# Optimization experiments

Measured on AMD Instinct MI355X. Metric: run time of the kernel, lower is better.

The kernel has to match this reference:

```python
import jax, jax.numpy as jnp
import numpy as np

B, S, D, H = 8, 1024, 1024, 16
DK = D // H
NEG = -1e9


def setup_inputs() -> dict:
    key = jax.random.key(0)
    ks = jax.random.split(key, 11)
    s = 1.0 / np.sqrt(D)
    inp = {
        "query": jax.random.normal(ks[0], (B, S, D), jnp.float32),
        "key": jax.random.normal(ks[1], (B, S, D), jnp.float32),
        "value": jax.random.normal(ks[2], (B, S, D), jnp.float32),
        "mask": jnp.tril(jnp.ones((S, S), jnp.int32))[None, None],  # causal [1,1,S,S]
        "w_q": jax.random.normal(ks[3], (D, D), jnp.float32) * s,
        "b_q": jnp.zeros((D,), jnp.float32),
        "w_k": jax.random.normal(ks[4], (D, D), jnp.float32) * s,
        "b_k": jnp.zeros((D,), jnp.float32),
        "w_v": jax.random.normal(ks[5], (D, D), jnp.float32) * s,
        "b_v": jnp.zeros((D,), jnp.float32),
        "w_o": jax.random.normal(ks[6], (D, D), jnp.float32) * s,
        "b_o": jnp.zeros((D,), jnp.float32),
    }
    return inp


def reference(query, key, value, mask, w_q, b_q, w_k, b_k, w_v, b_v, w_o, b_o):
    # projections; weights stored as [in, out] (torch Linear applies x @ W.T; here
    # we use x @ W which is the same math with W = torch_W.T)
    def proj(x, w, b):
        # [B,S,D] -> [B,H,S,DK]
        y = x @ w + b
        return y.reshape(B, S, H, DK).transpose(0, 2, 1, 3)

    q = proj(query, w_q, b_q)
    k = proj(key, w_k, b_k)
    v = proj(value, w_v, b_v)

    scores = jnp.einsum("bhqd,bhkd->bhqk", q, k) / jnp.sqrt(jnp.float32(DK))
    scores = jnp.where(mask == 0, jnp.float32(NEG), scores)
    probs = jax.nn.softmax(scores, axis=-1)
    # dropout: eval mode (identity) for deterministic reference
    ctx = jnp.einsum("bhqk,bhkd->bhqd", probs, v)
    ctx = ctx.transpose(0, 2, 1, 3).reshape(B, S, D)
    return ctx @ w_o + b_o
```

## Files before the change

kernel.cpp:

```cpp
#include <hip/hip_runtime.h>

#define B_ 8
#define S_ 1024
#define D_ 1024
#define H_ 16
#define DK_ 64
#define M_ (B_ * S_)
#define NEGINF -1e38f

typedef __bf16 bf16_t;
typedef __bf16 bf16x8 __attribute__((ext_vector_type(8)));
typedef float f32x4 __attribute__((ext_vector_type(4)));
typedef unsigned int u32;

__device__ inline f32x4 mfma_bf16(bf16x8 a, bf16x8 b, f32x4 c) {
    return __builtin_amdgcn_mfma_f32_16x16x32_bf16(a, b, c, 0, 0, 0);
}

typedef const __attribute__((address_space(1))) u32* gas1_t;
typedef __attribute__((address_space(3))) u32* las3_t;
__device__ inline void gl_lds16(const void* g, void* l) {
    __builtin_amdgcn_global_load_lds((gas1_t)g, (las3_t)l, 16, 0, 0);
}

__device__ inline bf16x8 load8(const bf16_t* p) { return *(const bf16x8*)p; }
__device__ inline bf16x8 load8(const float* p) {
    const f32x4 a = *(const f32x4*)p;
    const f32x4 b = *(const f32x4*)(p + 4);
    bf16x8 r;
    r[0] = (bf16_t)a[0]; r[1] = (bf16_t)a[1];
    r[2] = (bf16_t)a[2]; r[3] = (bf16_t)a[3];
    r[4] = (bf16_t)b[0]; r[5] = (bf16_t)b[1];
    r[6] = (bf16_t)b[2]; r[7] = (bf16_t)b[3];
    return r;
}
__device__ inline void store_elem(bf16_t* Y, size_t i, float v) { Y[i] = (bf16_t)v; }
__device__ inline void store_elem(float* Y, size_t i, float v) { Y[i] = v; }

__global__ __launch_bounds__(256) void transpose4(
    const float* __restrict__ i0, const float* __restrict__ i1,
    const float* __restrict__ i2, const float* __restrict__ i3,
    bf16_t* __restrict__ o0, bf16_t* __restrict__ o1,
    bf16_t* __restrict__ o2, bf16_t* __restrict__ o3) {
    const float* ins[4] = {i0, i1, i2, i3};
    bf16_t* outs[4] = {o0, o1, o2, o3};
    const float* in = ins[blockIdx.z];
    bf16_t* out = outs[blockIdx.z];
    __shared__ __align__(16) bf16_t t[32][33];
    const int n0 = blockIdx.x * 32, k0 = blockIdx.y * 32;
    const int tx = threadIdx.x;
    for (int i = threadIdx.y; i < 32; i += 8)
        t[i][tx] = (bf16_t)in[(size_t)(k0 + i) * D_ + n0 + tx];
    __syncthreads();
    for (int i = threadIdx.y; i < 32; i += 8)
        out[(size_t)(n0 + i) * D_ + k0 + tx] = t[tx][i];
}

__global__ __launch_bounds__(256) void cvt_bf16(const float* __restrict__ in,
                                                bf16_t* __restrict__ out,
                                                int n8) {
    const int i = blockIdx.x * 256 + threadIdx.x;
    if (i < n8) *(bf16x8*)(out + (size_t)i * 8) = load8(in + (size_t)i * 8);
}

template <int MODE, typename TX, typename TY>
__global__ __launch_bounds__(256) void gemm_bt(
    const TX* __restrict__ X, const bf16_t* __restrict__ Wt,
    const float* __restrict__ bias, TY* __restrict__ Y, float scale) {
    __shared__ __align__(16) bf16_t As[2][128 * 64];
    __shared__ __align__(16) bf16_t Bs[2][128 * 64];
    const int tid = threadIdx.x;
    const int lane = tid & 63, wave = tid >> 6;
    const int ln = lane & 15, quad = lane >> 4;
    const int wm = (wave & 1) * 64, wn = (wave >> 1) * 64;
    const int m0 = blockIdx.x * 128, n0 = blockIdx.y * 128;

    const int srow = tid >> 3;
    const int sch = tid & 7;
    const int swc = sch ^ (srow & 7);

    const TX* pa = X + (size_t)(m0 + srow) * D_ + swc * 8;
    const bf16_t* pb = Wt + (size_t)(n0 + srow) * D_ + swc * 8;

    auto stage = [&](int d, int k0) {
        if constexpr (sizeof(TX) == 2) {
#pragma unroll
            for (int i = 0; i < 4; i++)
                gl_lds16(pa + (size_t)(i * 32) * D_ + k0,
                         As[d] + i * 2048 + wave * 512);
        } else {
#pragma unroll
            for (int i = 0; i < 4; i++)
                *(bf16x8*)(As[d] + (srow + i * 32) * 64 + sch * 8) =
                    load8(X + (size_t)(m0 + srow + i * 32) * D_ + k0 + swc * 8);
        }
#pragma unroll
        for (int i = 0; i < 4; i++)
            gl_lds16(pb + (size_t)(i * 32) * D_ + k0,
                     Bs[d] + i * 2048 + wave * 512);
    };

    stage(0, 0);
    __syncthreads();

    f32x4 acc[4][4] = {};
    int cur = 0;
    for (int t = 0; t < 16; ++t) {
        if (t < 15) stage(cur ^ 1, (t + 1) * 64);
#pragma unroll
        for (int kq = 0; kq < 2; kq++) {
            bf16x8 af[4], bfr[4];
            const int slot = ((kq * 4 + quad) ^ (ln & 7)) * 8;
#pragma unroll
            for (int mt = 0; mt < 4; mt++)
                af[mt] =
                    *(const bf16x8*)(As[cur] + (wm + mt * 16 + ln) * 64 + slot);
#pragma unroll
            for (int nt = 0; nt < 4; nt++)
                bfr[nt] =
                    *(const bf16x8*)(Bs[cur] + (wn + nt * 16 + ln) * 64 + slot);
#pragma unroll
            for (int mt = 0; mt < 4; mt++)
#pragma unroll
                for (int nt = 0; nt < 4; nt++)
                    acc[mt][nt] = mfma_bf16(af[mt], bfr[nt], acc[mt][nt]);
        }
        __syncthreads();
        cur ^= 1;
    }

#pragma unroll
    for (int mt = 0; mt < 4; mt++) {
#pragma unroll
        for (int nt = 0; nt < 4; nt++) {
#pragma unroll
            for (int r = 0; r < 4; r++) {
                const int m = m0 + wm + mt * 16 + quad * 4 + r;
                const int n = n0 + wn + nt * 16 + ln;
                const float v = (acc[mt][nt][r] + bias[n]) * scale;
                size_t idx;
                if (MODE == 0) {
                    idx = (size_t)m * D_ + n;
                } else {
                    const int b = m >> 10, s = m & 1023;
                    const int h = n >> 6, d = n & 63;
                    if (MODE == 1)
                        idx = ((size_t)(b * H_ + h) * S_ + s) * DK_ + d;
                    else
                        idx = ((size_t)(b * H_ + h) * DK_ + d) * S_ + s;
                }
                store_elem(Y, idx, v);
            }
        }
    }
}

__global__ __launch_bounds__(256, 4) void MaskedMultiHeadAttention_90709709291709_kernel(
    const bf16_t* __restrict__ Q, const bf16_t* __restrict__ K,
    const bf16_t* __restrict__ Vt, bf16_t* __restrict__ ctx) {
    __shared__ __align__(16) bf16_t Ks[64 * 64];
    __shared__ __align__(16) bf16_t Vs[64 * 64];

    const int bh = blockIdx.x;
    const int j = 7 - (int)blockIdx.y;
    const int tid = threadIdx.x;
    const int lane = tid & 63, wave = tid >> 6;
    const int ln = lane & 15, quad = lane >> 4;

    const bf16_t* Qb = Q + (size_t)bh * S_ * DK_;
    const bf16_t* Kb = K + (size_t)bh * S_ * DK_;
    const bf16_t* Vb = Vt + (size_t)bh * DK_ * S_;
    const int b = bh >> 4, h = bh & 15;

    bf16x8 ones8;
#pragma unroll
    for (int i = 0; i < 8; i++) ones8[i] = (bf16_t)1.0f;

    const int qb = j * 128;
    const int wq = qb + wave * 32;

    bf16x8 qf[2][2];
#pragma unroll
    for (int mi = 0; mi < 2; mi++)
#pragma unroll
        for (int kk = 0; kk < 2; kk++)
            qf[mi][kk] = *(const bf16x8*)(
                Qb + (size_t)(wq + mi * 16 + ln) * DK_ + kk * 32 + quad * 8);

    f32x4 o[2][4] = {};
    f32x4 ol[2] = {};

    const int r8 = lane >> 3;
    const int sc = (lane & 7) ^ r8;

    const int kend = qb + 128;
    for (int kt = 0; kt < kend; kt += 64) {
#pragma unroll
        for (int i = 0; i < 2; i++) {
            const int g = wave * 2 + i;
            const int krow = (g & 2) * 16 + (g & 1) * 16 + (r8 & 4) * 2 +
                             (g & 4) + (r8 & 3);
            gl_lds16(Kb + (size_t)(kt + krow) * DK_ + sc * 8, Ks + g * 512);
            gl_lds16(Vb + (size_t)(g * 8 + r8) * S_ + kt + sc * 8,
                     Vs + g * 512);
        }
        __syncthreads();

        if (kt <= wq + 31) {
            bf16x8 pa[2][2];
#pragma unroll
            for (int mi = 0; mi < 2; mi++) {
                f32x4 s[4];
#pragma unroll
                for (int nt = 0; nt < 4; nt++) {
                    const bf16_t* kp = Ks + (nt * 16 + ln) * 64;
                    const bf16x8 kf0 =
                        *(const bf16x8*)(kp + ((quad ^ (ln & 7)) * 8));
                    const bf16x8 kf1 =
                        *(const bf16x8*)(kp + (((4 + quad) ^ (ln & 7)) * 8));
                    f32x4 a = {-16.f, -16.f, -16.f, -16.f};
                    a = mfma_bf16(kf0, qf[mi][0], a);
                    a = mfma_bf16(kf1, qf[mi][1], a);
                    s[nt] = a;
                }
                const int q = wq + mi * 16 + ln;
                const bool needmask = (kt + 63) > q;
#pragma unroll
                for (int nt = 0; nt < 4; nt++)
#pragma unroll
                    for (int r = 0; r < 4; r++) {
                        const int ktrue = kt + (nt & 1) * 32 + quad * 8 +
                                          (nt >> 1) * 4 + r;
                        float v = s[nt][r];
                        if (needmask && ktrue > q) v = NEGINF;
                        s[nt][r] = __builtin_amdgcn_exp2f(v);
                    }
#pragma unroll
                for (int kk = 0; kk < 2; kk++) {
                    bf16x8 t;
#pragma unroll
                    for (int w = 0; w < 4; w++) {
                        const int nts = 2 * (w >> 1) + kk;
                        const int r0 = 2 * (w & 1);
                        t[2 * w] = (bf16_t)s[nts][r0];
                        t[2 * w + 1] = (bf16_t)s[nts][r0 + 1];
                    }
                    pa[mi][kk] = t;
                }
                ol[mi] = mfma_bf16(pa[mi][0], ones8, ol[mi]);
                ol[mi] = mfma_bf16(pa[mi][1], ones8, ol[mi]);
            }
#pragma unroll
            for (int dk = 0; dk < 4; dk++) {
                const bf16_t* vp = Vs + (dk * 16 + ln) * 64;
                const bf16x8 vf0 = *(const bf16x8*)(vp + ((quad ^ (ln & 7)) * 8));
                const bf16x8 vf1 =
                    *(const bf16x8*)(vp + (((4 + quad) ^ (ln & 7)) * 8));
#pragma unroll
                for (int mi = 0; mi < 2; mi++) {
                    o[mi][dk] = mfma_bf16(pa[mi][0], vf0, o[mi][dk]);
                    o[mi][dk] = mfma_bf16(pa[mi][1], vf1, o[mi][dk]);
                }
            }
        }
        __syncthreads();
    }

#pragma unroll
    for (int mi = 0; mi < 2; mi++)
#pragma unroll
        for (int r = 0; r < 4; r++) {
            const float inv = 1.f / ol[mi][r];
            const int row = wq + mi * 16 + quad * 4 + r;
            const size_t base = ((size_t)b * S_ + row) * D_ + h * DK_;
#pragma unroll
            for (int dk = 0; dk < 4; dk++)
                ctx[base + dk * 16 + ln] = (bf16_t)(o[mi][dk][r] * inv);
        }
}

__global__ __launch_bounds__(256) void copy16(const f32x4* __restrict__ src,
                                              f32x4* __restrict__ dst, int n4) {
    const int i = blockIdx.x * 256 + threadIdx.x;
    if (i < n4) dst[i] = src[i];
}

extern "C" void kernel_launch(void* const* d_in, const int* in_sizes, int n_in,
                              void* d_out, int out_size, void* d_ws,
                              size_t ws_size, hipStream_t stream) {
    const float* query = (const float*)d_in[0];
    const float* key = (const float*)d_in[1];
    const float* value = (const float*)d_in[2];
    const float* w_q = (const float*)d_in[4];
    const float* b_q = (const float*)d_in[5];
    const float* w_k = (const float*)d_in[6];
    const float* b_k = (const float*)d_in[7];
    const float* w_v = (const float*)d_in[8];
    const float* b_v = (const float*)d_in[9];
    const float* w_o = (const float*)d_in[10];
    const float* b_o = (const float*)d_in[11];

    bf16_t* ws = (bf16_t*)d_ws;
    const size_t M8 = (size_t)M_ * D_;
    bf16_t* Qw = ws;
    bf16_t* Kw = ws + M8;
    bf16_t* Vw = ws + 2 * M8;
    bf16_t* wtq = ws + 3 * M8;
    bf16_t* wtk = wtq + (size_t)D_ * D_;
    bf16_t* wtv = wtk + (size_t)D_ * D_;
    bf16_t* wto = wtv + (size_t)D_ * D_;

    bf16_t* Xb = (bf16_t*)d_out;

    const size_t need_direct = (4 * M8 + 4 * (size_t)D_ * D_) * sizeof(bf16_t);
    const bool direct = ws_size >= need_direct;
    bf16_t* Cw = direct ? (ws + 3 * M8 + 4 * (size_t)D_ * D_)
                        : (bf16_t*)d_out;
    float* Yw = direct ? (float*)d_out : (float*)ws;

    transpose4<<<dim3(32, 32, 4), dim3(32, 8, 1), 0, stream>>>(
        w_q, w_k, w_v, w_o, wtq, wtk, wtv, wto);

    const dim3 gg(M_ / 128, D_ / 128, 1);
    const int n8 = (int)(M8 / 8);
    const dim3 gc((n8 + 255) / 256, 1, 1);
    const float qscale = 0.125f * 1.4426950408889634f;

    cvt_bf16<<<gc, 256, 0, stream>>>(query, Xb, n8);
    gemm_bt<1><<<gg, 256, 0, stream>>>(Xb, wtq, b_q, Qw, qscale);
    cvt_bf16<<<gc, 256, 0, stream>>>(key, Xb, n8);
    gemm_bt<1><<<gg, 256, 0, stream>>>(Xb, wtk, b_k, Kw, 1.0f);
    cvt_bf16<<<gc, 256, 0, stream>>>(value, Xb, n8);
    gemm_bt<2><<<gg, 256, 0, stream>>>(Xb, wtv, b_v, Vw, 1.0f);

    MaskedMultiHeadAttention_90709709291709_kernel<<<dim3(B_ * H_, 8, 1), 256,
                                                     0, stream>>>(Qw, Kw, Vw,
                                                                  Cw);

    gemm_bt<0><<<gg, 256, 0, stream>>>(Cw, wto, b_o, Yw, 1.0f);
    if (!direct) {
        const int n4 = (int)((M8 * 4) / 16);
        copy16<<<dim3((n4 + 255) / 256), 256, 0, stream>>>((const f32x4*)Yw,
                                                           (f32x4*)d_out, n4);
    }
}
```

Measured before the change: 309.7 us.

## Double-buffer K/V tiles in attention and batch input conversions into one launch

The attention kernel now keeps two LDS buffers for K/V tiles and prefetches the next tile while computing the current one, with one barrier per iteration. Causal masking is applied only on diagonal tiles, so off-diagonal tiles skip the per-element compare. When the workspace is large enough, the three fp32-to-bf16 conversions run as a single 3D launch into separate buffers, cutting two kernel launches. The second LDS buffer doubles shared memory use, which may lower occupancy, and the fast path needs a larger workspace.

```diff
diff --git a/kernel.cpp b/kernel.cpp
--- a/kernel.cpp
+++ b/kernel.cpp
@@ -63,6 +63,18 @@
     if (i < n8) *(bf16x8*)(out + (size_t)i * 8) = load8(in + (size_t)i * 8);
 }
 
+__global__ __launch_bounds__(256) void cvt_bf16_3(
+    const float* __restrict__ iq, const float* __restrict__ ik,
+    const float* __restrict__ iv, bf16_t* __restrict__ oq,
+    bf16_t* __restrict__ ok, bf16_t* __restrict__ ov, int n8) {
+    const float* ins[3] = {iq, ik, iv};
+    bf16_t* outs[3] = {oq, ok, ov};
+    const float* in = ins[blockIdx.z];
+    bf16_t* out = outs[blockIdx.z];
+    const int i = blockIdx.x * 256 + threadIdx.x;
+    if (i < n8) *(bf16x8*)(out + (size_t)i * 8) = load8(in + (size_t)i * 8);
+}
+
 template <int MODE, typename TX, typename TY>
 __global__ __launch_bounds__(256) void gemm_bt(
     const TX* __restrict__ X, const bf16_t* __restrict__ Wt,
@@ -158,8 +170,8 @@
 __global__ __launch_bounds__(256, 4) void MaskedMultiHeadAttention_90709709291709_kernel(
     const bf16_t* __restrict__ Q, const bf16_t* __restrict__ K,
     const bf16_t* __restrict__ Vt, bf16_t* __restrict__ ctx) {
-    __shared__ __align__(16) bf16_t Ks[64 * 64];
-    __shared__ __align__(16) bf16_t Vs[64 * 64];
+    __shared__ __align__(16) bf16_t Ks[2][64 * 64];
+    __shared__ __align__(16) bf16_t Vs[2][64 * 64];
 
     const int bh = blockIdx.x;
     const int j = 7 - (int)blockIdx.y;
@@ -192,28 +204,39 @@
 
     const int r8 = lane >> 3;
     const int sc = (lane & 7) ^ r8;
-
-    const int kend = qb + 128;
-    for (int kt = 0; kt < kend; kt += 64) {
-#pragma unroll
-        for (int i = 0; i < 2; i++) {
-            const int g = wave * 2 + i;
-            const int krow = (g & 2) * 16 + (g & 1) * 16 + (r8 & 4) * 2 +
-                             (g & 4) + (r8 & 3);
-            gl_lds16(Kb + (size_t)(kt + krow) * DK_ + sc * 8, Ks + g * 512);
-            gl_lds16(Vb + (size_t)(g * 8 + r8) * S_ + kt + sc * 8,
-                     Vs + g * 512);
-        }
-        __syncthreads();
+    const int g0 = wave * 2, g1 = wave * 2 + 1;
+    const int krow0 = (g0 & 2) * 16 + (g0 & 1) * 16 + (r8 & 4) * 2 + (g0 & 4) +
+                      (r8 & 3);
+    const int krow1 = (g1 & 2) * 16 + (g1 & 1) * 16 + (r8 & 4) * 2 + (g1 & 4) +
+                      (r8 & 3);
+    const int vrow0 = g0 * 8 + r8, vrow1 = g1 * 8 + r8;
+
+    const int ntile = (qb + 128) >> 6;
+
+    auto stageT = [&](int d, int kt) {
+        gl_lds16(Kb + (size_t)(kt + krow0) * DK_ + sc * 8, Ks[d] + g0 * 512);
+        gl_lds16(Kb + (size_t)(kt + krow1) * DK_ + sc * 8, Ks[d] + g1 * 512);
+        gl_lds16(Vb + (size_t)vrow0 * S_ + kt + sc * 8, Vs[d] + g0 * 512);
+        gl_lds16(Vb + (size_t)vrow1 * S_ + kt + sc * 8, Vs[d] + g1 * 512);
+    };
+
+    stageT(0, 0);
+    __syncthreads();
+
+    int cur = 0;
+    for (int t = 0; t < ntile; ++t) {
+        const int kt = t * 64;
+        if (t + 1 < ntile) stageT(cur ^ 1, kt + 64);
 
         if (kt <= wq + 31) {
+            const bool diag = (kt + 64 > wq);
             bf16x8 pa[2][2];
 #pragma unroll
             for (int mi = 0; mi < 2; mi++) {
                 f32x4 s[4];
 #pragma unroll
                 for (int nt = 0; nt < 4; nt++) {
-                    const bf16_t* kp = Ks + (nt * 16 + ln) * 64;
+                    const bf16_t* kp = Ks[cur] + (nt * 16 + ln) * 64;
                     const bf16x8 kf0 =
                         *(const bf16x8*)(kp + ((quad ^ (ln & 7)) * 8));
                     const bf16x8 kf1 =
@@ -223,37 +246,45 @@
                     a = mfma_bf16(kf1, qf[mi][1], a);
                     s[nt] = a;
                 }
-                const int q = wq + mi * 16 + ln;
-                const bool needmask = (kt + 63) > q;
-#pragma unroll
-                for (int nt = 0; nt < 4; nt++)
-#pragma unroll
-                    for (int r = 0; r < 4; r++) {
-                        const int ktrue = kt + (nt & 1) * 32 + quad * 8 +
-                                          (nt >> 1) * 4 + r;
-                        float v = s[nt][r];
-                        if (needmask && ktrue > q) v = NEGINF;
-                        s[nt][r] = __builtin_amdgcn_exp2f(v);
-                    }
+                if (diag) {
+                    const int q = wq + mi * 16 + ln;
+#pragma unroll
+                    for (int nt = 0; nt < 4; nt++)
+#pragma unroll
+                        for (int r = 0; r < 4; r++) {
+                            const int ktrue = kt + (nt & 1) * 32 + quad * 8 +
+                                              (nt >> 1) * 4 + r;
+                            float v = s[nt][r];
+                            if (ktrue > q) v = NEGINF;
+                            s[nt][r] = __builtin_amdgcn_exp2f(v);
+                        }
+                } else {
+#pragma unroll
+                    for (int nt = 0; nt < 4; nt++)
+#pragma unroll
+                        for (int r = 0; r < 4; r++)
+                            s[nt][r] = __builtin_amdgcn_exp2f(s[nt][r]);
+                }
 #pragma unroll
                 for (int kk = 0; kk < 2; kk++) {
-                    bf16x8 t;
+                    bf16x8 tpk;
 #pragma unroll
                     for (int w = 0; w < 4; w++) {
                         const int nts = 2 * (w >> 1) + kk;
                         const int r0 = 2 * (w & 1);
-                        t[2 * w] = (bf16_t)s[nts][r0];
-                        t[2 * w + 1] = (bf16_t)s[nts][r0 + 1];
+                        tpk[2 * w] = (bf16_t)s[nts][r0];
+                        tpk[2 * w + 1] = (bf16_t)s[nts][r0 + 1];
                     }
-                    pa[mi][kk] = t;
+                    pa[mi][kk] = tpk;
                 }
                 ol[mi] = mfma_bf16(pa[mi][0], ones8, ol[mi]);
                 ol[mi] = mfma_bf16(pa[mi][1], ones8, ol[mi]);
             }
 #pragma unroll
             for (int dk = 0; dk < 4; dk++) {
-                const bf16_t* vp = Vs + (dk * 16 + ln) * 64;
-                const bf16x8 vf0 = *(const bf16x8*)(vp + ((quad ^ (ln & 7)) * 8));
+                const bf16_t* vp = Vs[cur] + (dk * 16 + ln) * 64;
+                const bf16x8 vf0 =
+                    *(const bf16x8*)(vp + ((quad ^ (ln & 7)) * 8));
                 const bf16x8 vf1 =
                     *(const bf16x8*)(vp + (((4 + quad) ^ (ln & 7)) * 8));
 #pragma unroll
@@ -264,6 +295,7 @@
             }
         }
         __syncthreads();
+        cur ^= 1;
     }
 
 #pragma unroll
@@ -302,45 +334,65 @@
 
     bf16_t* ws = (bf16_t*)d_ws;
     const size_t M8 = (size_t)M_ * D_;
+    const size_t DD = (size_t)D_ * D_;
     bf16_t* Qw = ws;
     bf16_t* Kw = ws + M8;
     bf16_t* Vw = ws + 2 * M8;
     bf16_t* wtq = ws + 3 * M8;
-    bf16_t* wtk = wtq + (size_t)D_ * D_;
-    bf16_t* wtv = wtk + (size_t)D_ * D_;
-    bf16_t* wto = wtv + (size_t)D_ * D_;
-
-    bf16_t* Xb = (bf16_t*)d_out;
-
-    const size_t need_direct = (4 * M8 + 4 * (size_t)D_ * D_) * sizeof(bf16_t);
-    const bool direct = ws_size >= need_direct;
-    bf16_t* Cw = direct ? (ws + 3 * M8 + 4 * (size_t)D_ * D_)
-                        : (bf16_t*)d_out;
-    float* Yw = direct ? (float*)d_out : (float*)ws;
+    bf16_t* wtk = wtq + DD;
+    bf16_t* wtv = wtk + DD;
+    bf16_t* wto = wtv + DD;
+
+    const int n8 = (int)(M8 / 8);
+    const dim3 gg(M_ / 128, D_ / 128, 1);
+    const float qscale = 0.125f * 1.4426950408889634f;
 
     transpose4<<<dim3(32, 32, 4), dim3(32, 8, 1), 0, stream>>>(
         w_q, w_k, w_v, w_o, wtq, wtk, wtv, wto);
 
-    const dim3 gg(M_ / 128, D_ / 128, 1);
-    const int n8 = (int)(M8 / 8);
-    const dim3 gc((n8 + 255) / 256, 1, 1);
-    const float qscale = 0.125f * 1.4426950408889634f;
-
-    cvt_bf16<<<gc, 256, 0, stream>>>(query, Xb, n8);
-    gemm_bt<1><<<gg, 256, 0, stream>>>(Xb, wtq, b_q, Qw, qscale);
-    cvt_bf16<<<gc, 256, 0, stream>>>(key, Xb, n8);
-    gemm_bt<1><<<gg, 256, 0, stream>>>(Xb, wtk, b_k, Kw, 1.0f);
-    cvt_bf16<<<gc, 256, 0, stream>>>(value, Xb, n8);
-    gemm_bt<2><<<gg, 256, 0, stream>>>(Xb, wtv, b_v, Vw, 1.0f);
-
-    MaskedMultiHeadAttention_90709709291709_kernel<<<dim3(B_ * H_, 8, 1), 256,
-                                                     0, stream>>>(Qw, Kw, Vw,
-                                                                  Cw);
-
-    gemm_bt<0><<<gg, 256, 0, stream>>>(Cw, wto, b_o, Yw, 1.0f);
-    if (!direct) {
-        const int n4 = (int)((M8 * 4) / 16);
-        copy16<<<dim3((n4 + 255) / 256), 256, 0, stream>>>((const f32x4*)Yw,
-                                                           (f32x4*)d_out, n4);
+    const size_t need_big = (7 * M8 + 4 * DD) * sizeof(bf16_t);
+    if (ws_size >= need_big) {
+        bf16_t* Xq = ws + 3 * M8 + 4 * DD;
+        bf16_t* Xk = Xq + M8;
+        bf16_t* Xv = Xk + M8;
+        bf16_t* Cw = Xv + M8;
+        float* Yw = (float*)d_out;
+
+        cvt_bf16_3<<<dim3((n8 + 255) / 256, 1, 3), 256, 0, stream>>>(
+            query, key, value, Xq, Xk, Xv, n8);
+        gemm_bt<1><<<gg, 256, 0, stream>>>(Xq, wtq, b_q, Qw, qscale);
+        gemm_bt<1><<<gg, 256, 0, stream>>>(Xk, wtk, b_k, Kw, 1.0f);
+        gemm_bt<2><<<gg, 256, 0, stream>>>(Xv, wtv, b_v, Vw, 1.0f);
+
+        MaskedMultiHeadAttention_90709709291709_kernel<<<dim3(B_ * H_, 8, 1),
+                                                         256, 0, stream>>>(
+            Qw, Kw, Vw, Cw);
+
+        gemm_bt<0><<<gg, 256, 0, stream>>>(Cw, wto, b_o, Yw, 1.0f);
+    } else {
+        bf16_t* Xb = (bf16_t*)d_out;
+        const size_t need_direct = (4 * M8 + 4 * DD) * sizeof(bf16_t);
+        const bool direct = ws_size >= need_direct;
+        bf16_t* Cw = direct ? (ws + 3 * M8 + 4 * DD) : (bf16_t*)d_out;
+        float* Yw = direct ? (float*)d_out : (float*)ws;
+        const dim3 gc((n8 + 255) / 256, 1, 1);
+
+        cvt_bf16<<<gc, 256, 0, stream>>>(query, Xb, n8);
+        gemm_bt<1><<<gg, 256, 0, stream>>>(Xb, wtq, b_q, Qw, qscale);
+        cvt_bf16<<<gc, 256, 0, stream>>>(key, Xb, n8);
+        gemm_bt<1><<<gg, 256, 0, stream>>>(Xb, wtk, b_k, Kw, 1.0f);
+        cvt_bf16<<<gc, 256, 0, stream>>>(value, Xb, n8);
+        gemm_bt<2><<<gg, 256, 0, stream>>>(Xb, wtv, b_v, Vw, 1.0f);
+
+        MaskedMultiHeadAttention_90709709291709_kernel<<<dim3(B_ * H_, 8, 1),
+                                                         256, 0, stream>>>(
+            Qw, Kw, Vw, Cw);
+
+        gemm_bt<0><<<gg, 256, 0, stream>>>(Cw, wto, b_o, Yw, 1.0f);
+        if (!direct) {
+            const int n4 = (int)((M8 * 4) / 16);
+            copy16<<<dim3((n4 + 255) / 256), 256, 0, stream>>>(
+                (const f32x4*)Yw, (f32x4*)d_out, n4);
+        }
     }
 }
```

New measurement: 323.6 us. +4.5%, slower.

## Batch QKV conversion and projections into single prep and GEMM launches

Applied to the files above, without the earlier changes.

Weight transposes and the three fp32-to-bf16 input conversions are merged into one prep kernel. The three projection GEMMs become one launch with a z-dimension selecting Q, K or V. This cuts launches from seven to two and gives each GEMM launch three times as many blocks, which helps fill the GPU. It needs a larger workspace for three separate bf16 input buffers and falls back to the old sequential path when the workspace is too small.

```diff
diff --git a/kernel.cpp b/kernel.cpp
--- a/kernel.cpp
+++ b/kernel.cpp
@@ -37,23 +37,36 @@
 __device__ inline void store_elem(bf16_t* Y, size_t i, float v) { Y[i] = (bf16_t)v; }
 __device__ inline void store_elem(float* Y, size_t i, float v) { Y[i] = v; }
 
-__global__ __launch_bounds__(256) void transpose4(
-    const float* __restrict__ i0, const float* __restrict__ i1,
-    const float* __restrict__ i2, const float* __restrict__ i3,
-    bf16_t* __restrict__ o0, bf16_t* __restrict__ o1,
-    bf16_t* __restrict__ o2, bf16_t* __restrict__ o3) {
-    const float* ins[4] = {i0, i1, i2, i3};
-    bf16_t* outs[4] = {o0, o1, o2, o3};
-    const float* in = ins[blockIdx.z];
-    bf16_t* out = outs[blockIdx.z];
+__global__ __launch_bounds__(256) void prep(
+    const float* __restrict__ wq, const float* __restrict__ wk,
+    const float* __restrict__ wv, const float* __restrict__ wo,
+    bf16_t* __restrict__ wt,
+    const float* __restrict__ q, const float* __restrict__ k,
+    const float* __restrict__ v,
+    bf16_t* __restrict__ X,
+    int n8) {
+    const int z = blockIdx.z;
+    const int tid = threadIdx.x;
     __shared__ __align__(16) bf16_t t[32][33];
-    const int n0 = blockIdx.x * 32, k0 = blockIdx.y * 32;
-    const int tx = threadIdx.x;
-    for (int i = threadIdx.y; i < 32; i += 8)
-        t[i][tx] = (bf16_t)in[(size_t)(k0 + i) * D_ + n0 + tx];
-    __syncthreads();
-    for (int i = threadIdx.y; i < 32; i += 8)
-        out[(size_t)(n0 + i) * D_ + k0 + tx] = t[tx][i];
+    if (z < 4) {
+        if (blockIdx.x >= 1024) return;
+        const float* ins[4] = {wq, wk, wv, wo};
+        const float* in = ins[z];
+        bf16_t* out = wt + (size_t)z * D_ * D_;
+        const int n0 = (blockIdx.x & 31) * 32, k0 = ((int)blockIdx.x >> 5) * 32;
+        const int tx = tid & 31, ty = tid >> 5;
+        for (int i = ty; i < 32; i += 8)
+            t[i][tx] = (bf16_t)in[(size_t)(k0 + i) * D_ + n0 + tx];
+        __syncthreads();
+        for (int i = ty; i < 32; i += 8)
+            out[(size_t)(n0 + i) * D_ + k0 + tx] = t[tx][i];
+    } else {
+        const float* ins[3] = {q, k, v};
+        const float* in = ins[z - 4];
+        bf16_t* out = X + (size_t)(z - 4) * M_ * D_;
+        const int i = blockIdx.x * 256 + tid;
+        if (i < n8) *(bf16x8*)(out + (size_t)i * 8) = load8(in + (size_t)i * 8);
+    }
 }
 
 __global__ __launch_bounds__(256) void cvt_bf16(const float* __restrict__ in,
@@ -61,6 +74,109 @@
                                                 int n8) {
     const int i = blockIdx.x * 256 + threadIdx.x;
     if (i < n8) *(bf16x8*)(out + (size_t)i * 8) = load8(in + (size_t)i * 8);
+}
+
+template <typename TX>
+__device__ inline void gemm_core(const TX* __restrict__ X,
+                                 const bf16_t* __restrict__ Wt, int m0, int n0,
+                                 bf16_t (*As)[128 * 64], bf16_t (*Bs)[128 * 64],
+                                 f32x4 acc[4][4]) {
+    const int tid = threadIdx.x;
+    const int lane = tid & 63, wave = tid >> 6;
+    const int ln = lane & 15, quad = lane >> 4;
+    const int wm = (wave & 1) * 64, wn = (wave >> 1) * 64;
+
+    const int srow = tid >> 3;
+    const int sch = tid & 7;
+    const int swc = sch ^ (srow & 7);
+
+    const TX* pa = X + (size_t)(m0 + srow) * D_ + swc * 8;
+    const bf16_t* pb = Wt + (size_t)(n0 + srow) * D_ + swc * 8;
+
+    auto stage = [&](int d, int k0) {
+        if constexpr (sizeof(TX) == 2) {
+#pragma unroll
+            for (int i = 0; i < 4; i++)
+                gl_lds16(pa + (size_t)(i * 32) * D_ + k0,
+                         As[d] + i * 2048 + wave * 512);
+        } else {
+#pragma unroll
+            for (int i = 0; i < 4; i++)
+                *(bf16x8*)(As[d] + (srow + i * 32) * 64 + sch * 8) =
+                    load8(X + (size_t)(m0 + srow + i * 32) * D_ + k0 + swc * 8);
+        }
+#pragma unroll
+        for (int i = 0; i < 4; i++)
+            gl_lds16(pb + (size_t)(i * 32) * D_ + k0,
+                     Bs[d] + i * 2048 + wave * 512);
+    };
+
+    stage(0, 0);
+    __syncthreads();
+
+    int cur = 0;
+    for (int t = 0; t < 16; ++t) {
+        if (t < 15) stage(cur ^ 1, (t + 1) * 64);
+#pragma unroll
+        for (int kq = 0; kq < 2; kq++) {
+            bf16x8 af[4], bfr[4];
+            const int slot = ((kq * 4 + quad) ^ (ln & 7)) * 8;
+#pragma unroll
+            for (int mt = 0; mt < 4; mt++)
+                af[mt] =
+                    *(const bf16x8*)(As[cur] + (wm + mt * 16 + ln) * 64 + slot);
+#pragma unroll
+            for (int nt = 0; nt < 4; nt++)
+                bfr[nt] =
+                    *(const bf16x8*)(Bs[cur] + (wn + nt * 16 + ln) * 64 + slot);
+#pragma unroll
+            for (int mt = 0; mt < 4; mt++)
+#pragma unroll
+                for (int nt = 0; nt < 4; nt++)
+                    acc[mt][nt] = mfma_bf16(af[mt], bfr[nt], acc[mt][nt]);
+        }
+        __syncthreads();
+        cur ^= 1;
+    }
+}
+
+__global__ __launch_bounds__(256) void gemm_qkv(
+    const bf16_t* __restrict__ Xbase, const bf16_t* __restrict__ Wtbase,
+    const float* __restrict__ bq, const float* __restrict__ bk,
+    const float* __restrict__ bv, bf16_t* __restrict__ Ybase, float qscale) {
+    __shared__ __align__(16) bf16_t As[2][128 * 64];
+    __shared__ __align__(16) bf16_t Bs[2][128 * 64];
+    const int z = blockIdx.z;
+    const bf16_t* X = Xbase + (size_t)z * M_ * D_;
+    const bf16_t* Wt = Wtbase + (size_t)z * D_ * D_;
+    const float* bias = z == 0 ? bq : (z == 1 ? bk : bv);
+    bf16_t* Y = Ybase + (size_t)z * M_ * D_;
+    const float scale = z == 0 ? qscale : 1.0f;
+    const int m0 = blockIdx.x * 128, n0 = blockIdx.y * 128;
+
+    f32x4 acc[4][4] = {};
+    gemm_core(X, Wt, m0, n0, As, Bs, acc);
+
+    const int tid = threadIdx.x;
+    const int lane = tid & 63, wave = tid >> 6;
+    const int ln = lane & 15, quad = lane >> 4;
+    const int wm = (wave & 1) * 64, wn = (wave >> 1) * 64;
+#pragma unroll
+    for (int mt = 0; mt < 4; mt++)
+#pragma unroll
+        for (int nt = 0; nt < 4; nt++)
+#pragma unroll
+            for (int r = 0; r < 4; r++) {
+                const int m = m0 + wm + mt * 16 + quad * 4 + r;
+                const int n = n0 + wn + nt * 16 + ln;
+                const float v = (acc[mt][nt][r] + bias[n]) * scale;
+                const int b = m >> 10, s = m & 1023;
+                const int h = n >> 6, d = n & 63;
+                const size_t idx =
+                    (z == 2) ? ((size_t)(b * H_ + h) * DK_ + d) * S_ + s
+                             : ((size_t)(b * H_ + h) * S_ + s) * DK_ + d;
+                Y[idx] = (bf16_t)v;
+            }
 }
 
 template <int MODE, typename TX, typename TY>
@@ -69,70 +185,19 @@
     const float* __restrict__ bias, TY* __restrict__ Y, float scale) {
     __shared__ __align__(16) bf16_t As[2][128 * 64];
     __shared__ __align__(16) bf16_t Bs[2][128 * 64];
+    const int m0 = blockIdx.x * 128, n0 = blockIdx.y * 128;
+
+    f32x4 acc[4][4] = {};
+    gemm_core(X, Wt, m0, n0, As, Bs, acc);
+
     const int tid = threadIdx.x;
     const int lane = tid & 63, wave = tid >> 6;
     const int ln = lane & 15, quad = lane >> 4;
     const int wm = (wave & 1) * 64, wn = (wave >> 1) * 64;
-    const int m0 = blockIdx.x * 128, n0 = blockIdx.y * 128;
-
-    const int srow = tid >> 3;
-    const int sch = tid & 7;
-    const int swc = sch ^ (srow & 7);
-
-    const TX* pa = X + (size_t)(m0 + srow) * D_ + swc * 8;
-    const bf16_t* pb = Wt + (size_t)(n0 + srow) * D_ + swc * 8;
-
-    auto stage = [&](int d, int k0) {
-        if constexpr (sizeof(TX) == 2) {
-#pragma unroll
-            for (int i = 0; i < 4; i++)
-                gl_lds16(pa + (size_t)(i * 32) * D_ + k0,
-                         As[d] + i * 2048 + wave * 512);
-        } else {
-#pragma unroll
-            for (int i = 0; i < 4; i++)
-                *(bf16x8*)(As[d] + (srow + i * 32) * 64 + sch * 8) =
-                    load8(X + (size_t)(m0 + srow + i * 32) * D_ + k0 + swc * 8);
-        }
-#pragma unroll
-        for (int i = 0; i < 4; i++)
-            gl_lds16(pb + (size_t)(i * 32) * D_ + k0,
-                     Bs[d] + i * 2048 + wave * 512);
-    };
-
-    stage(0, 0);
-    __syncthreads();
-
-    f32x4 acc[4][4] = {};
-    int cur = 0;
-    for (int t = 0; t < 16; ++t) {
-        if (t < 15) stage(cur ^ 1, (t + 1) * 64);
-#pragma unroll
-        for (int kq = 0; kq < 2; kq++) {
-            bf16x8 af[4], bfr[4];
-            const int slot = ((kq * 4 + quad) ^ (ln & 7)) * 8;
-#pragma unroll
-            for (int mt = 0; mt < 4; mt++)
-                af[mt] =
-                    *(const bf16x8*)(As[cur] + (wm + mt * 16 + ln) * 64 + slot);
-#pragma unroll
-            for (int nt = 0; nt < 4; nt++)
-                bfr[nt] =
-                    *(const bf16x8*)(Bs[cur] + (wn + nt * 16 + ln) * 64 + slot);
-#pragma unroll
-            for (int mt = 0; mt < 4; mt++)
-#pragma unroll
-                for (int nt = 0; nt < 4; nt++)
-                    acc[mt][nt] = mfma_bf16(af[mt], bfr[nt], acc[mt][nt]);
-        }
-        __syncthreads();
-        cur ^= 1;
-    }
-
-#pragma unroll
-    for (int mt = 0; mt < 4; mt++) {
-#pragma unroll
-        for (int nt = 0; nt < 4; nt++) {
+#pragma unroll
+    for (int mt = 0; mt < 4; mt++)
+#pragma unroll
+        for (int nt = 0; nt < 4; nt++)
 #pragma unroll
             for (int r = 0; r < 4; r++) {
                 const int m = m0 + wm + mt * 16 + quad * 4 + r;
@@ -151,8 +216,6 @@
                 }
                 store_elem(Y, idx, v);
             }
-        }
-    }
 }
 
 __global__ __launch_bounds__(256, 4) void MaskedMultiHeadAttention_90709709291709_kernel(
@@ -302,45 +365,61 @@
 
     bf16_t* ws = (bf16_t*)d_ws;
     const size_t M8 = (size_t)M_ * D_;
+    const size_t DD = (size_t)D_ * D_;
     bf16_t* Qw = ws;
     bf16_t* Kw = ws + M8;
     bf16_t* Vw = ws + 2 * M8;
     bf16_t* wtq = ws + 3 * M8;
-    bf16_t* wtk = wtq + (size_t)D_ * D_;
-    bf16_t* wtv = wtk + (size_t)D_ * D_;
-    bf16_t* wto = wtv + (size_t)D_ * D_;
-
-    bf16_t* Xb = (bf16_t*)d_out;
-
-    const size_t need_direct = (4 * M8 + 4 * (size_t)D_ * D_) * sizeof(bf16_t);
-    const bool direct = ws_size >= need_direct;
-    bf16_t* Cw = direct ? (ws + 3 * M8 + 4 * (size_t)D_ * D_)
-                        : (bf16_t*)d_out;
-    float* Yw = direct ? (float*)d_out : (float*)ws;
-
-    transpose4<<<dim3(32, 32, 4), dim3(32, 8, 1), 0, stream>>>(
-        w_q, w_k, w_v, w_o, wtq, wtk, wtv, wto);
-
+    bf16_t* wtk = wtq + DD;
+    bf16_t* wtv = wtk + DD;
+    bf16_t* wto = wtv + DD;
+
+    const int n8 = (int)(M8 / 8);
     const dim3 gg(M_ / 128, D_ / 128, 1);
-    const int n8 = (int)(M8 / 8);
-    const dim3 gc((n8 + 255) / 256, 1, 1);
     const float qscale = 0.125f * 1.4426950408889634f;
 
-    cvt_bf16<<<gc, 256, 0, stream>>>(query, Xb, n8);
-    gemm_bt<1><<<gg, 256, 0, stream>>>(Xb, wtq, b_q, Qw, qscale);
-    cvt_bf16<<<gc, 256, 0, stream>>>(key, Xb, n8);
-    gemm_bt<1><<<gg, 256, 0, stream>>>(Xb, wtk, b_k, Kw, 1.0f);
-    cvt_bf16<<<gc, 256, 0, stream>>>(value, Xb, n8);
-    gemm_bt<2><<<gg, 256, 0, stream>>>(Xb, wtv, b_v, Vw, 1.0f);
-
-    MaskedMultiHeadAttention_90709709291709_kernel<<<dim3(B_ * H_, 8, 1), 256,
-                                                     0, stream>>>(Qw, Kw, Vw,
-                                                                  Cw);
-
-    gemm_bt<0><<<gg, 256, 0, stream>>>(Cw, wto, b_o, Yw, 1.0f);
-    if (!direct) {
-        const int n4 = (int)((M8 * 4) / 16);
-        copy16<<<dim3((n4 + 255) / 256), 256, 0, stream>>>((const f32x4*)Yw,
-                                                           (f32x4*)d_out, n4);
+    const size_t need_big = (7 * M8 + 4 * DD) * sizeof(bf16_t);
+    if (ws_size >= need_big) {
+        bf16_t* Xq = ws + 3 * M8 + 4 * DD;
+        bf16_t* Cw = Xq + 3 * M8;
+        float* Yw = (float*)d_out;
+
+        prep<<<dim3(4096, 1, 7), 256, 0, stream>>>(
+            w_q, w_k, w_v, w_o, wtq, query, key, value, Xq, n8);
+        gemm_qkv<<<dim3(M_ / 128, D_ / 128, 3), 256, 0, stream>>>(
+            Xq, wtq, b_q, b_k, b_v, Qw, qscale);
+
+        MaskedMultiHeadAttention_90709709291709_kernel<<<dim3(B_ * H_, 8, 1),
+                                                         256, 0, stream>>>(
+            Qw, Kw, Vw, Cw);
+
+        gemm_bt<0><<<gg, 256, 0, stream>>>(Cw, wto, b_o, Yw, 1.0f);
+    } else {
+        bf16_t* Xb = (bf16_t*)d_out;
+        const size_t need_direct = (4 * M8 + 4 * DD) * sizeof(bf16_t);
+        const bool direct = ws_size >= need_direct;
+        bf16_t* Cw = direct ? (ws + 3 * M8 + 4 * DD) : (bf16_t*)d_out;
+        float* Yw = direct ? (float*)d_out : (float*)ws;
+        const dim3 gc((n8 + 255) / 256, 1, 1);
+
+        prep<<<dim3(1024, 1, 4), 256, 0, stream>>>(
+            w_q, w_k, w_v, w_o, wtq, nullptr, nullptr, nullptr, nullptr, 0);
+        cvt_bf16<<<gc, 256, 0, stream>>>(query, Xb, n8);
+        gemm_bt<1><<<gg, 256, 0, stream>>>(Xb, wtq, b_q, Qw, qscale);
+        cvt_bf16<<<gc, 256, 0, stream>>>(key, Xb, n8);
+        gemm_bt<1><<<gg, 256, 0, stream>>>(Xb, wtk, b_k, Kw, 1.0f);
+        cvt_bf16<<<gc, 256, 0, stream>>>(value, Xb, n8);
+        gemm_bt<2><<<gg, 256, 0, stream>>>(Xb, wtv, b_v, Vw, 1.0f);
+
+        MaskedMultiHeadAttention_90709709291709_kernel<<<dim3(B_ * H_, 8, 1),
+                                                         256, 0, stream>>>(
+            Qw, Kw, Vw, Cw);
+
+        gemm_bt<0><<<gg, 256, 0, stream>>>(Cw, wto, b_o, Yw, 1.0f);
+        if (!direct) {
+            const int n4 = (int)((M8 * 4) / 16);
+            copy16<<<dim3((n4 + 255) / 256), 256, 0, stream>>>(
+                (const f32x4*)Yw, (f32x4*)d_out, n4);
+        }
     }
 }
```

Result: no change. 309.6 us (-0.0%).
